# Kernel tuning notes

Measured on AMD Instinct MI355X. Metric: run time of the kernel, lower is better.

The kernel has to match this reference:

```python
import jax, jax.numpy as jnp
import numpy as np

N_WAY, K_SHOT, PRJ, D, H, W, Q = 5, 5, 14, 64, 10, 10, 1024
RATIOS = (0.25, 0.5, 0.75)
LAMDA = 32.0
MARGIN = 0.3


def _l2norm(x, axis):
    return x / jnp.maximum(jnp.linalg.norm(x, axis=axis, keepdims=True), 1e-12)


def _cos(a, b, axis=-1, eps=1e-8):
    num = (a * b).sum(axis)
    na = jnp.maximum(jnp.linalg.norm(a, axis=axis), eps)
    nb = jnp.maximum(jnp.linalg.norm(b, axis=axis), eps)
    return num / (na * nb)


def setup_inputs() -> dict:
    key = jax.random.key(0)
    ks = jax.random.split(key, 6)
    feat = jax.random.normal(ks[0], (N_WAY * K_SHOT * PRJ + Q, D, H, W), jnp.float32)
    label = jax.random.randint(ks[1], (Q,), 0, N_WAY)
    Wq = jax.random.normal(ks[2], (D, D // 4), jnp.float32) * 0.05
    bq = jnp.zeros((D // 4,), jnp.float32)
    Wk = jax.random.normal(ks[3], (D, D // 4), jnp.float32) * 0.05
    bk = jnp.zeros((D // 4,), jnp.float32)
    temperature = jnp.ones((), jnp.float32)
    gate_logits = jnp.zeros((len(RATIOS),), jnp.float32)
    return {"feat": feat, "temperature": temperature, "gate_logits": gate_logits,
            "Wq": Wq, "bq": bq, "Wk": Wk, "bk": bk, "label": label}


def reference(feat, temperature, gate_logits, Wq, bq, Wk, bk, label):
    ns = N_WAY * K_SHOT * PRJ
    support = _l2norm(feat[:ns], 1).reshape(N_WAY, K_SHOT, PRJ, D, H * W)
    query = _l2norm(feat[ns:], 1)                       # [Q, D, H, W]
    view_proto = support.mean(1)                        # [n, v, d, hw]
    q_flat = query.reshape(query.shape[0], -1)          # [Q, D*H*W]
    vf = _l2norm(view_proto.reshape(N_WAY, PRJ, -1), -1)
    # per-view similarity (vectorized over the 14-view python loop)
    sim_all = jnp.einsum('qf,nvf->qnv', q_flat, vf) / (temperature + 1e-6)
    p_w = jax.nn.softmax(sim_all, -1)                   # [Q, n, v]
    # softmax-weighted multi-view prototype fusion (replaces batched loops)
    proto_q = jnp.einsum('qnv,nvdh->qndh', p_w, view_proto)  # [Q, n, d, hw]
    spatial_attn = jax.nn.sigmoid(proto_q.mean(2, keepdims=True))
    proto_q = (proto_q * spatial_attn).sum(-1)          # [Q, n, d]
    query_vec = query.mean((2, 3))                      # [Q, d]
    # qpa align loss
    cos = _cos(query_vec[:, None, :], proto_q)          # [Q, n]
    pos_mask = jax.nn.one_hot(label, N_WAY, dtype=cos.dtype)
    pos_sim = (cos * pos_mask).sum(-1)
    neg = jnp.where(pos_mask > 0, -jnp.inf, cos)
    hardest_neg = jax.lax.top_k(neg, min(3, N_WAY - 1))[0].mean(-1)
    align_loss = jnp.maximum(hardest_neg - pos_sim + MARGIN, 0.0).mean()
    # QSA mini cross-attention
    qp = query_vec @ Wq + bq                            # [Q, D/4]
    kp = proto_q @ Wk + bk                              # [Q, n, D/4]
    scale = jnp.sqrt(jnp.asarray(D // 4, cos.dtype))
    attn = jax.nn.softmax(jnp.einsum('qe,qne->qn', qp, kp) / scale, -1)
    fused = proto_q * attn[..., None]                   # [Q, n, d]
    # DeltaGate: topk delta + multi-ratio soft mask
    base = view_proto.mean((1, 3))                      # [n, d]
    delta = jnp.abs(fused - base[None])
    Ks = [max(1, int(r * D)) for r in RATIOS]
    max_K = max(Ks)
    idx = jax.lax.top_k(delta, max_K)[1]                # [Q, n, max_K]
    mode_w = jax.nn.softmax(gate_logits)
    ranks = jnp.arange(max_K)
    rank_w = sum(mode_w[i] * (ranks < Ks[i]).astype(delta.dtype) for i in range(len(Ks)))
    combined = jnp.einsum('qnkd,k->qnd', jax.nn.one_hot(idx, D, dtype=delta.dtype), rank_w)
    gated = _l2norm(fused * combined, -1)
    cos2 = _cos(query_vec[:, None, :], gated)           # [Q, n]
    # AIS classification loss (source unavailable; faithful surrogate: scaled CE)
    logp = jax.nn.log_softmax(LAMDA * cos2, -1)
    cls_loss = -(logp * pos_mask).sum(-1).mean()
    total_loss = cls_loss + 0.3 * align_loss
    pred = jax.nn.softmax(cos2, -1)
    return pred, total_loss
```

## Files before the change

kernel.cpp:

```cpp
#include <hip/hip_runtime.h>
#include <math.h>

#define NWAY 5
#define KSHOT 5
#define PRJ 14
#define DD 64
#define PP 100
#define NQ 1024
#define NS 350
#define NPAIR 70
#define LAMDA 32.0f
#define MARGIN 0.3f
#define PCHUNK 25
#define FGROUPS 25
#define KCH 256

#define VPT_OFF   0
#define VPTS_OFF  448000
#define B2T_OFF   2688000
#define MM_OFF    3136000
#define VNINV_OFF 3143000
#define PSUM_OFF  3143128
#define QV_OFF    3147608
#define SIM32_OFF 3315544
#define PW_OFF    7903064
#define PQ4_OFF   7974744
#define CLS_OFF   9285464
#define ALN_OFF   9286488
#define PSUMP_OFF 9287512
#define SSQP_OFF  9399512
#define FQBF_OFF  9401344

#define PQ_ELEMS (NQ*NWAY*64)
#define SIM_STRIDE (NQ*NPAIR)

typedef __attribute__((ext_vector_type(8))) short short8;
typedef __attribute__((ext_vector_type(4))) float f32x4;

__device__ __forceinline__ float redsum64(float x){
  #pragma unroll
  for (int o = 1; o < 64; o <<= 1) x += __shfl_xor(x, o, 64);
  return x;
}

__device__ __forceinline__ unsigned short bfr(float x){
  unsigned int u = __float_as_uint(x);
  unsigned int r = (u + 0x7FFFu + ((u >> 16) & 1u)) >> 16;
  return (unsigned short)r;
}

__global__ __launch_bounds__(256) void kN(const float* __restrict__ feat,
                                          float* __restrict__ vptS,
                                          float* __restrict__ qv,
                                          unsigned short* __restrict__ fqb){
  __shared__ float lds[64*101];
  __shared__ float inv[100];
  int s = blockIdx.x, t = threadIdx.x;
  const float* fp = feat + (size_t)s * 6400;
  #pragma unroll
  for (int i = 0; i < 25; i++){
    int j = t + 256*i;
    int d = j / 100, p = j - d*100;
    lds[d*101 + p] = fp[j];
  }
  __syncthreads();
  if (t < 100){
    float ss = 0.f;
    #pragma unroll
    for (int d = 0; d < 64; d++){ float x = lds[d*101 + t]; ss += x*x; }
    inv[t] = 1.f / fmaxf(sqrtf(ss), 1e-12f);
  }
  __syncthreads();
  if (s < NS){
    #pragma unroll
    for (int i = 0; i < 25; i++){
      int j = t + 256*i;
      int p = j >> 6, d = j & 63;
      vptS[(size_t)s*6400 + j] = lds[d*101 + p] * inv[p];
    }
  } else {
    int q = s - NS;
    #pragma unroll
    for (int i = 0; i < 25; i++){
      int j = t + 256*i;
      int d = j / 100, p = j - d*100;
      fqb[(size_t)q*6400 + j] = bfr(lds[d*101 + p] * inv[p]);
    }
    if (t < 64){
      float sum = 0.f;
      for (int p = 0; p < PP; p++) sum += lds[t*101 + p] * inv[p];
      qv[q*64 + t] = sum * 0.01f;
    }
  }
}

__global__ __launch_bounds__(256) void kVb(const float* __restrict__ vptS,
                                           float* __restrict__ vpt,
                                           unsigned short* __restrict__ B2T,
                                           float* __restrict__ MM,
                                           float* __restrict__ psumP,
                                           float* __restrict__ ssqP){
  __shared__ float l2[256];
  __shared__ float wssq[4];
  int b = blockIdx.x;
  int pair = b / 25, jc = b - pair*25;
  int n = pair / PRJ, v = pair - n*PRJ;
  int j0 = jc * 256;
  int t = threadIdx.x;
  int j = j0 + t;
  float s = 0.f;
  #pragma unroll
  for (int k = 0; k < KSHOT; k++){
    int sk = (n*KSHOT + k)*PRJ + v;
    s += vptS[(size_t)sk*6400 + j];
  }
  float val = s * 0.2f;
  vpt[(size_t)pair*6400 + j] = val;
  int p = j >> 6, d = j & 63;
  int plocal = p & 3;
  l2[d*4 + plocal] = val;
  float sq = redsum64(val*val);
  if ((t & 63) == 0) wssq[t >> 6] = sq;
  __syncthreads();
  if (t < 64){
    int p0 = j0 >> 6;
    float4 w4 = make_float4(l2[t*4+0], l2[t*4+1], l2[t*4+2], l2[t*4+3]);
    ushort4 h;
    h.x = bfr(w4.x); h.y = bfr(w4.y); h.z = bfr(w4.z); h.w = bfr(w4.w);
    *(ushort4*)(B2T + (size_t)pair*6400 + t*100 + p0) = h;
    psumP[((size_t)pair*25 + jc)*64 + t] = w4.x + w4.y + w4.z + w4.w;
  }
  if (t >= 128 && t < 132){
    int i = t - 128;
    float m = 0.f;
    #pragma unroll
    for (int dd2 = 0; dd2 < 64; dd2++) m += l2[dd2*4 + i];
    MM[pair*100 + (j0 >> 6) + i] = m * (1.f/64.f);
  }
  if (t == 192)
    ssqP[pair*25 + jc] = wssq[0] + wssq[1] + wssq[2] + wssq[3];
}

__global__ __launch_bounds__(64) void kVc2(const float* __restrict__ psumP,
                                           const float* __restrict__ ssqP,
                                           float* __restrict__ psum,
                                           float* __restrict__ vninv){
  int pair = blockIdx.x, l = threadIdx.x;
  float s = 0.f;
  #pragma unroll
  for (int c = 0; c < 25; c++) s += psumP[((size_t)pair*25 + c)*64 + l];
  psum[pair*64 + l] = s;
  float sq = (l < 25) ? ssqP[pair*25 + l] : 0.f;
  float tot = redsum64(sq);
  if (l == 0) vninv[pair] = 1.f / fmaxf(sqrtf(tot), 1e-12f);
}

__global__ __launch_bounds__(256) void kS(const unsigned short* __restrict__ fqb,
                                          const unsigned short* __restrict__ B2T,
                                          float* __restrict__ sim32){
  int b = blockIdx.x;
  int fg = b % FGROUPS, mg = b / FGROUPS;
  int t = threadIdx.x;
  int l = t & 63;
  int wu = __builtin_amdgcn_readfirstlane(t >> 6);
  int q0 = mg*64 + wu*16;
  int fbase = fg * KCH;

  int lr = l & 15;
  int kb = l >> 4;

  f32x4 acc0 = {0.f,0.f,0.f,0.f};
  f32x4 acc1 = {0.f,0.f,0.f,0.f};
  f32x4 acc2 = {0.f,0.f,0.f,0.f};
  f32x4 acc3 = {0.f,0.f,0.f,0.f};
  f32x4 acc4 = {0.f,0.f,0.f,0.f};

  const unsigned short* Ab = fqb + (size_t)(q0 + lr)*6400 + fbase + kb*8;
  const unsigned short* Bb = B2T + (size_t)lr*6400 + fbase + kb*8;
  bool ok4 = (64 + lr) < NPAIR;

  #pragma unroll
  for (int s = 0; s < 8; s++){
    short8 a = *(const short8*)(Ab + s*32);
    short8 b0 = *(const short8*)(Bb + s*32);
    short8 b1 = *(const short8*)(Bb + 16*6400 + s*32);
    short8 b2 = *(const short8*)(Bb + 32*6400 + s*32);
    short8 b3 = *(const short8*)(Bb + 48*6400 + s*32);
    short8 b4 = ok4 ? *(const short8*)(Bb + (size_t)64*6400 + s*32) : (short8)(short)0;
    acc0 = __builtin_amdgcn_mfma_f32_16x16x32_bf16(a, b0, acc0, 0, 0, 0);
    acc1 = __builtin_amdgcn_mfma_f32_16x16x32_bf16(a, b1, acc1, 0, 0, 0);
    acc2 = __builtin_amdgcn_mfma_f32_16x16x32_bf16(a, b2, acc2, 0, 0, 0);
    acc3 = __builtin_amdgcn_mfma_f32_16x16x32_bf16(a, b3, acc3, 0, 0, 0);
    acc4 = __builtin_amdgcn_mfma_f32_16x16x32_bf16(a, b4, acc4, 0, 0, 0);
  }

  float* sp = sim32 + (size_t)fg*SIM_STRIDE + (size_t)(q0 + kb*4)*NPAIR;
  #pragma unroll
  for (int i = 0; i < 4; i++){
    sp[(size_t)i*NPAIR + lr]      = acc0[i];
    sp[(size_t)i*NPAIR + 16 + lr] = acc1[i];
    sp[(size_t)i*NPAIR + 32 + lr] = acc2[i];
    sp[(size_t)i*NPAIR + 48 + lr] = acc3[i];
    if (ok4) sp[(size_t)i*NPAIR + 64 + lr] = acc4[i];
  }
}

__global__ __launch_bounds__(256) void kM(const float* __restrict__ sim32,
                                          const float* __restrict__ vninv,
                                          const float* __restrict__ temp,
                                          float* __restrict__ pw){
  int t = blockIdx.x*256 + threadIdx.x;
  if (t >= NQ*NWAY) return;
  int q = t / NWAY, n = t - q*NWAY;
  float invT = 1.f / (temp[0] + 1e-6f);
  float s[PRJ];
  #pragma unroll
  for (int v = 0; v < PRJ; v++) s[v] = 0.f;
  for (int c = 0; c < FGROUPS; c++){
    const float* sp = sim32 + (size_t)c*SIM_STRIDE + q*NPAIR + n*PRJ;
    #pragma unroll
    for (int v = 0; v < PRJ; v++) s[v] += sp[v];
  }
  float m = -3.4e38f;
  #pragma unroll
  for (int v = 0; v < PRJ; v++){
    s[v] = s[v] * vninv[n*PRJ + v] * invT;
    m = fmaxf(m, s[v]);
  }
  float sum = 0.f;
  #pragma unroll
  for (int v = 0; v < PRJ; v++){ s[v] = expf(s[v] - m); sum += s[v]; }
  float rs = 1.f / sum;
  #pragma unroll
  for (int v = 0; v < PRJ; v++) pw[q*NPAIR + n*PRJ + v] = s[v] * rs;
}

__global__ __launch_bounds__(256) void kP(const float* __restrict__ vpt,
                                          const float* __restrict__ pw,
                                          const float* __restrict__ MM,
                                          float* __restrict__ pq4){
  __shared__ float sgl[16][PCHUNK];
  int b = blockIdx.x;
  int n  = b / 256;
  int r  = b - n*256;
  int qb = r >> 2;
  int s  = r & 3;
  int p0 = s * PCHUNK;
  int t = threadIdx.x, w = t >> 6, l = t & 63;
  int q0 = qb*16 + w*4;

  float wq[4][PRJ];
  #pragma unroll
  for (int j = 0; j < 4; j++)
    #pragma unroll
    for (int v = 0; v < PRJ; v++)
      wq[j][v] = pw[(q0+j)*NPAIR + n*PRJ + v];

  if (l < PCHUNK){
    #pragma unroll
    for (int j = 0; j < 4; j++){
      float ssg = 0.f;
      #pragma unroll
      for (int v = 0; v < PRJ; v++)
        ssg += wq[j][v] * MM[(n*PRJ + v)*100 + p0 + l];
      sgl[w*4 + j][l] = 1.f / (1.f + expf(-ssg));
    }
  }
  __syncthreads();

  float acc[4] = {0.f, 0.f, 0.f, 0.f};
  const float* vb = vpt + (size_t)n * PRJ * 6400;
  for (int pl = 0; pl < PCHUNK; pl++){
    int p = p0 + pl;
    float vv[PRJ];
    #pragma unroll
    for (int v = 0; v < PRJ; v++) vv[v] = vb[v*6400 + p*64 + l];
    #pragma unroll
    for (int j = 0; j < 4; j++){
      float dot = 0.f;
      #pragma unroll
      for (int v = 0; v < PRJ; v++) dot += wq[j][v] * vv[v];
      acc[j] += sgl[w*4 + j][pl] * dot;
    }
  }
  #pragma unroll
  for (int j = 0; j < 4; j++)
    pq4[(size_t)s*PQ_ELEMS + ((q0+j)*NWAY + n)*64 + l] = acc[j];
}

__global__ __launch_bounds__(320) void kF(const float* __restrict__ qv,
                                          const float* __restrict__ pq4,
                                          const float* __restrict__ psum,
                                          const float* __restrict__ Wq,
                                          const float* __restrict__ bq,
                                          const float* __restrict__ Wk,
                                          const float* __restrict__ bk,
                                          const float* __restrict__ gate,
                                          const int*   __restrict__ label,
                                          float* __restrict__ pred,
                                          float* __restrict__ cls,
                                          float* __restrict__ aln){
  __shared__ float qvl[64];
  __shared__ float qp[16];
  __shared__ float scn[NWAY], cosn[NWAY], c2n[NWAY];
  __shared__ float dl5[NWAY][64];
  int q = blockIdx.x, t = threadIdx.x;
  int w = t >> 6, l = t & 63;

  float qvv = qv[q*64 + l];
  float qss = redsum64(qvv*qvv);
  float qn8 = fmaxf(sqrtf(qss), 1e-8f);
  if (w == 0) qvl[l] = qvv;
  __syncthreads();
  if (w == 0 && l < 16){
    float s = bq[l];
    #pragma unroll
    for (int d = 0; d < 64; d++) s += qvl[d] * Wq[d*16 + l];
    qp[l] = s;
  }
  __syncthreads();

  float wkq = 0.f;
  #pragma unroll
  for (int e = 0; e < 16; e++) wkq += Wk[l*16 + e] * qp[e];
  float qpb = 0.f;
  #pragma unroll
  for (int e = 0; e < 16; e++) qpb += qp[e] * bk[e];

  size_t idx = (size_t)(q*NWAY + w)*64 + l;
  float x = pq4[idx] + pq4[PQ_ELEMS + idx] + pq4[2*PQ_ELEMS + idx] + pq4[3*PQ_ELEMS + idx];

  float dq = redsum64(qvv * x);
  float ps = redsum64(x * x);
  float cosw = dq / (qn8 * fmaxf(sqrtf(ps), 1e-8f));
  float sd = redsum64(x * wkq);
  float scw = (sd + qpb) * 0.25f;
  if (l == 0){ scn[w] = scw; cosn[w] = cosw; }
  __syncthreads();

  float am = scn[0];
  #pragma unroll
  for (int n = 1; n < NWAY; n++) am = fmaxf(am, scn[n]);
  float asum = 0.f;
  #pragma unroll
  for (int n = 0; n < NWAY; n++) asum += expf(scn[n] - am);
  float attw = expf(scw - am) / asum;

  float g0 = gate[0], g1 = gate[1], g2 = gate[2];
  float gm = fmaxf(fmaxf(g0, g1), g2);
  float e0 = expf(g0 - gm), e1 = expf(g1 - gm), e2 = expf(g2 - gm);
  float gs = 1.f / (e0 + e1 + e2);
  float b0 = (e0 + e1 + e2) * gs;
  float b1 = (e1 + e2) * gs;
  float b2 = e2 * gs;

  float bs = 0.f;
  #pragma unroll
  for (int v = 0; v < PRJ; v++) bs += psum[(w*PRJ + v)*64 + l];
  bs *= (1.f/1400.f);

  float f  = x * attw;
  float dd = fabsf(f - bs);
  dl5[w][l] = dd;
  int rank = 0;
  #pragma unroll 8
  for (int j = 0; j < 64; j++){
    float dj = dl5[w][j];
    rank += (dj > dd) || (dj == dd && j < l);
  }
  float cw = (rank < 16) ? b0 : (rank < 32) ? b1 : (rank < 48) ? b2 : 0.f;
  float gl = f * cw;
  float gss = redsum64(gl * gl);
  float num = redsum64(qvv * gl);
  float c2w = num / (qn8 * fmaxf(sqrtf(gss), 1e-12f));
  if (l == 0) c2n[w] = c2w;
  __syncthreads();

  float mx = c2n[0];
  #pragma unroll
  for (int n = 1; n < NWAY; n++) mx = fmaxf(mx, c2n[n]);
  float psum2 = 0.f;
  #pragma unroll
  for (int n = 0; n < NWAY; n++) psum2 += expf(c2n[n] - mx);
  if (l == 0) pred[q*NWAY + w] = expf(c2w - mx) / psum2;

  if (t == 0){
    int lab = label[q];
    float lm = LAMDA * mx;
    float lsum = 0.f;
    #pragma unroll
    for (int n = 0; n < NWAY; n++) lsum += expf(LAMDA * c2n[n] - lm);
    float c2l = c2n[lab], cosl = cosn[lab];
    float clsv = (lm + logf(lsum)) - LAMDA * c2l;
    float sum5 = 0.f, minn = 3.4e38f;
    #pragma unroll
    for (int n = 0; n < NWAY; n++){
      sum5 += cosn[n];
      if (n != lab) minn = fminf(minn, cosn[n]);
    }
    float hn = (sum5 - cosl - minn) * (1.f/3.f);
    float al = fmaxf(hn - cosl + MARGIN, 0.f);
    cls[q] = clsv; aln[q] = al;
  }
}

__global__ __launch_bounds__(256) void kL(const float* __restrict__ cls,
                                          const float* __restrict__ aln,
                                          float* __restrict__ out){
  __shared__ float r1[256], r2[256];
  int t = threadIdx.x;
  float s1 = 0.f, s2 = 0.f;
  for (int i = t; i < NQ; i += 256){ s1 += cls[i]; s2 += aln[i]; }
  r1[t] = s1; r2[t] = s2;
  __syncthreads();
  for (int o = 128; o > 0; o >>= 1){
    if (t < o){ r1[t] += r1[t + o]; r2[t] += r2[t + o]; }
    __syncthreads();
  }
  if (t == 0)
    out[NQ*NWAY] = r1[0]*(1.f/NQ) + 0.3f*(r2[0]*(1.f/NQ));
}

extern "C" void kernel_launch(void* const* d_in, const int* in_sizes, int n_in,
                              void* d_out, int out_size, void* d_ws, size_t ws_size,
                              hipStream_t stream){
  const float* feat = (const float*)d_in[0];
  const float* temp = (const float*)d_in[1];
  const float* gate = (const float*)d_in[2];
  const float* Wq   = (const float*)d_in[3];
  const float* bq   = (const float*)d_in[4];
  const float* Wk   = (const float*)d_in[5];
  const float* bk   = (const float*)d_in[6];
  const int*   lab  = (const int*)d_in[7];
  float* out = (float*)d_out;
  float* ws  = (float*)d_ws;

  float* vpt   = ws + VPT_OFF;
  float* vptS  = ws + VPTS_OFF;
  unsigned short* B2T = (unsigned short*)(ws + B2T_OFF);
  float* MMp   = ws + MM_OFF;
  float* vninv = ws + VNINV_OFF;
  float* psum  = ws + PSUM_OFF;
  float* qv    = ws + QV_OFF;
  float* sim32 = ws + SIM32_OFF;
  float* pw    = ws + PW_OFF;
  float* pq4   = ws + PQ4_OFF;
  float* cls   = ws + CLS_OFF;
  float* aln   = ws + ALN_OFF;
  float* psumP = ws + PSUMP_OFF;
  float* ssqP  = ws + SSQP_OFF;
  unsigned short* fqb = (unsigned short*)(ws + FQBF_OFF);

  hipLaunchKernelGGL(kN, dim3(NS + NQ), dim3(256), 0, stream, feat, vptS, qv, fqb);
  hipLaunchKernelGGL(kVb, dim3(NPAIR*25), dim3(256), 0, stream, vptS, vpt, B2T, MMp, psumP, ssqP);
  hipLaunchKernelGGL(kVc2, dim3(NPAIR), dim3(64), 0, stream, psumP, ssqP, psum, vninv);
  hipLaunchKernelGGL(kS, dim3(16*FGROUPS), dim3(256), 0, stream, fqb, B2T, sim32);
  hipLaunchKernelGGL(kM, dim3((NQ*NWAY + 255)/256), dim3(256), 0, stream, sim32, vninv, temp, pw);
  hipLaunchKernelGGL(kP, dim3(NWAY*256), dim3(256), 0, stream, vpt, pw, MMp, pq4);
  hipLaunchKernelGGL(kF, dim3(NQ), dim3(320), 0, stream, qv, pq4, psum, Wq, bq, Wk, bk, gate, lab, out, cls, aln);
  hipLaunchKernelGGL(kL, dim3(1), dim3(256), 0, stream, cls, aln, out);
}
```

Measured before the change: 90.92 us.

## Replace scalar prototype fusion kernel with bf16 MFMA GEMM and precomputed sigmoid gates

The scalar FP32 kP kernel, which computed softmax-weighted, sigmoid-gated prototype sums, is split into two kernels. kSg precomputes the per-query spatial sigmoid gates. kG recasts the fusion as a bf16 MFMA 16x16x32 matmul over a (view, position) reduction axis, using a new padded bf16 copy of the view prototypes (vptA) that kVb writes. The fp32 vpt buffer is dropped and partial outputs fall from 4 to 2 chunks. This trades an extra launch and a gate buffer round trip for matrix-core throughput, and adds bf16 rounding on both operands.

```diff
diff --git a/kernel.cpp b/kernel.cpp
--- a/kernel.cpp
+++ b/kernel.cpp
@@ -11,11 +11,9 @@
 #define NPAIR 70
 #define LAMDA 32.0f
 #define MARGIN 0.3f
-#define PCHUNK 25
 #define FGROUPS 25
 #define KCH 256
 
-#define VPT_OFF   0
 #define VPTS_OFF  448000
 #define B2T_OFF   2688000
 #define MM_OFF    3136000
@@ -24,12 +22,14 @@
 #define QV_OFF    3147608
 #define SIM32_OFF 3315544
 #define PW_OFF    7903064
-#define PQ4_OFF   7974744
+#define PQ2_OFF   7974744
 #define CLS_OFF   9285464
 #define ALN_OFF   9286488
 #define PSUMP_OFF 9287512
 #define SSQP_OFF  9399512
 #define FQBF_OFF  9401344
+#define VPTA_OFF  12678144
+#define SG_OFF    12964864
 
 #define PQ_ELEMS (NQ*NWAY*64)
 #define SIM_STRIDE (NQ*NPAIR)
@@ -95,8 +95,8 @@
 }
 
 __global__ __launch_bounds__(256) void kVb(const float* __restrict__ vptS,
-                                           float* __restrict__ vpt,
                                            unsigned short* __restrict__ B2T,
+                                           unsigned short* __restrict__ vptA,
                                            float* __restrict__ MM,
                                            float* __restrict__ psumP,
                                            float* __restrict__ ssqP){
@@ -115,9 +115,8 @@
     s += vptS[(size_t)sk*6400 + j];
   }
   float val = s * 0.2f;
-  vpt[(size_t)pair*6400 + j] = val;
-  int p = j >> 6, d = j & 63;
-  int plocal = p & 3;
+  int plocal = (j >> 6) & 3;
+  int d = j & 63;
   l2[d*4 + plocal] = val;
   float sq = redsum64(val*val);
   if ((t & 63) == 0) wssq[t >> 6] = sq;
@@ -128,6 +127,13 @@
     ushort4 h;
     h.x = bfr(w4.x); h.y = bfr(w4.y); h.z = bfr(w4.z); h.w = bfr(w4.w);
     *(ushort4*)(B2T + (size_t)pair*6400 + t*100 + p0) = h;
+    unsigned short* va = vptA + ((size_t)(n*64 + t))*1792 + v*128;
+    *(ushort4*)(va + p0) = h;
+    if (jc == 24){
+      #pragma unroll
+      for (int z = 0; z < 7; z++)
+        *(ushort4*)(va + 100 + z*4) = make_ushort4(0,0,0,0);
+    }
     psumP[((size_t)pair*25 + jc)*64 + t] = w4.x + w4.y + w4.z + w4.w;
   }
   if (t >= 128 && t < 132){
@@ -235,61 +241,76 @@
   for (int v = 0; v < PRJ; v++) pw[q*NPAIR + n*PRJ + v] = s[v] * rs;
 }
 
-__global__ __launch_bounds__(256) void kP(const float* __restrict__ vpt,
-                                          const float* __restrict__ pw,
-                                          const float* __restrict__ MM,
-                                          float* __restrict__ pq4){
-  __shared__ float sgl[16][PCHUNK];
-  int b = blockIdx.x;
-  int n  = b / 256;
-  int r  = b - n*256;
-  int qb = r >> 2;
-  int s  = r & 3;
-  int p0 = s * PCHUNK;
-  int t = threadIdx.x, w = t >> 6, l = t & 63;
-  int q0 = qb*16 + w*4;
-
-  float wq[4][PRJ];
-  #pragma unroll
-  for (int j = 0; j < 4; j++)
-    #pragma unroll
-    for (int v = 0; v < PRJ; v++)
-      wq[j][v] = pw[(q0+j)*NPAIR + n*PRJ + v];
-
-  if (l < PCHUNK){
-    #pragma unroll
-    for (int j = 0; j < 4; j++){
-      float ssg = 0.f;
+__global__ __launch_bounds__(256) void kSg(const float* __restrict__ pw,
+                                           const float* __restrict__ MM,
+                                           float* __restrict__ sg){
+  __shared__ float pwl[70];
+  int q = blockIdx.x, t = threadIdx.x;
+  if (t < NPAIR) pwl[t] = pw[q*NPAIR + t];
+  __syncthreads();
+  for (int i = t; i < NWAY*128; i += 256){
+    int n = i >> 7, p = i & 127;
+    float val = 0.f;
+    if (p < 100){
+      float s = 0.f;
       #pragma unroll
       for (int v = 0; v < PRJ; v++)
-        ssg += wq[j][v] * MM[(n*PRJ + v)*100 + p0 + l];
-      sgl[w*4 + j][l] = 1.f / (1.f + expf(-ssg));
-    }
-  }
-  __syncthreads();
-
-  float acc[4] = {0.f, 0.f, 0.f, 0.f};
-  const float* vb = vpt + (size_t)n * PRJ * 6400;
-  for (int pl = 0; pl < PCHUNK; pl++){
-    int p = p0 + pl;
-    float vv[PRJ];
-    #pragma unroll
-    for (int v = 0; v < PRJ; v++) vv[v] = vb[v*6400 + p*64 + l];
-    #pragma unroll
-    for (int j = 0; j < 4; j++){
-      float dot = 0.f;
-      #pragma unroll
-      for (int v = 0; v < PRJ; v++) dot += wq[j][v] * vv[v];
-      acc[j] += sgl[w*4 + j][pl] * dot;
-    }
-  }
-  #pragma unroll
-  for (int j = 0; j < 4; j++)
-    pq4[(size_t)s*PQ_ELEMS + ((q0+j)*NWAY + n)*64 + l] = acc[j];
+        s += pwl[n*PRJ + v] * MM[(n*PRJ + v)*100 + p];
+      val = 1.f / (1.f + expf(-s));
+    }
+    sg[(size_t)q*640 + i] = val;
+  }
+}
+
+__global__ __launch_bounds__(256) void kG(const float* __restrict__ sg,
+                                          const float* __restrict__ pw,
+                                          const unsigned short* __restrict__ vptA,
+                                          float* __restrict__ pq2){
+  int b = blockIdx.x;
+  int kh = b & 1;
+  int r = b >> 1;
+  int n = r / 64, qg = r - n*64;
+  int q0 = qg * 16;
+  int t = threadIdx.x;
+  int l = t & 63;
+  int wu = __builtin_amdgcn_readfirstlane(t >> 6);
+  int d0 = wu * 16;
+  int lr = l & 15, kb = l >> 4;
+
+  int q = q0 + lr;
+  const float* sgp = sg + (size_t)q*640 + n*128 + kb*8;
+  const unsigned short* Yb = vptA + ((size_t)(n*64 + d0 + lr))*1792 + kh*896 + kb*8;
+
+  float pv[7];
+  #pragma unroll
+  for (int i = 0; i < 7; i++) pv[i] = pw[q*NPAIR + n*PRJ + kh*7 + i];
+
+  f32x4 acc = {0.f,0.f,0.f,0.f};
+  #pragma unroll 4
+  for (int s = 0; s < 28; s++){
+    int pidx = (s & 3) * 32;
+    float4 g0 = *(const float4*)(sgp + pidx);
+    float4 g1 = *(const float4*)(sgp + pidx + 4);
+    float pwv = pv[s >> 2];
+    short8 a;
+    a[0] = (short)bfr(pwv * g0.x);
+    a[1] = (short)bfr(pwv * g0.y);
+    a[2] = (short)bfr(pwv * g0.z);
+    a[3] = (short)bfr(pwv * g0.w);
+    a[4] = (short)bfr(pwv * g1.x);
+    a[5] = (short)bfr(pwv * g1.y);
+    a[6] = (short)bfr(pwv * g1.z);
+    a[7] = (short)bfr(pwv * g1.w);
+    short8 y = *(const short8*)(Yb + s*32);
+    acc = __builtin_amdgcn_mfma_f32_16x16x32_bf16(a, y, acc, 0, 0, 0);
+  }
+  #pragma unroll
+  for (int i = 0; i < 4; i++)
+    pq2[(size_t)kh*PQ_ELEMS + ((size_t)(q0 + kb*4 + i)*NWAY + n)*64 + d0 + lr] = acc[i];
 }
 
 __global__ __launch_bounds__(320) void kF(const float* __restrict__ qv,
-                                          const float* __restrict__ pq4,
+                                          const float* __restrict__ pq2,
                                           const float* __restrict__ psum,
                                           const float* __restrict__ Wq,
                                           const float* __restrict__ bq,
@@ -328,7 +349,7 @@
   for (int e = 0; e < 16; e++) qpb += qp[e] * bk[e];
 
   size_t idx = (size_t)(q*NWAY + w)*64 + l;
-  float x = pq4[idx] + pq4[PQ_ELEMS + idx] + pq4[2*PQ_ELEMS + idx] + pq4[3*PQ_ELEMS + idx];
+  float x = pq2[idx] + pq2[(size_t)PQ_ELEMS + idx];
 
   float dq = redsum64(qvv * x);
   float ps = redsum64(x * x);
@@ -435,7 +456,6 @@
   float* out = (float*)d_out;
   float* ws  = (float*)d_ws;
 
-  float* vpt   = ws + VPT_OFF;
   float* vptS  = ws + VPTS_OFF;
   unsigned short* B2T = (unsigned short*)(ws + B2T_OFF);
   float* MMp   = ws + MM_OFF;
@@ -444,19 +464,22 @@
   float* qv    = ws + QV_OFF;
   float* sim32 = ws + SIM32_OFF;
   float* pw    = ws + PW_OFF;
-  float* pq4   = ws + PQ4_OFF;
+  float* pq2   = ws + PQ2_OFF;
   float* cls   = ws + CLS_OFF;
   float* aln   = ws + ALN_OFF;
   float* psumP = ws + PSUMP_OFF;
   float* ssqP  = ws + SSQP_OFF;
-  unsigned short* fqb = (unsigned short*)(ws + FQBF_OFF);
+  unsigned short* fqb  = (unsigned short*)(ws + FQBF_OFF);
+  unsigned short* vptA = (unsigned short*)(ws + VPTA_OFF);
+  float* sg    = ws + SG_OFF;
 
   hipLaunchKernelGGL(kN, dim3(NS + NQ), dim3(256), 0, stream, feat, vptS, qv, fqb);
-  hipLaunchKernelGGL(kVb, dim3(NPAIR*25), dim3(256), 0, stream, vptS, vpt, B2T, MMp, psumP, ssqP);
+  hipLaunchKernelGGL(kVb, dim3(NPAIR*25), dim3(256), 0, stream, vptS, B2T, vptA, MMp, psumP, ssqP);
   hipLaunchKernelGGL(kVc2, dim3(NPAIR), dim3(64), 0, stream, psumP, ssqP, psum, vninv);
   hipLaunchKernelGGL(kS, dim3(16*FGROUPS), dim3(256), 0, stream, fqb, B2T, sim32);
   hipLaunchKernelGGL(kM, dim3((NQ*NWAY + 255)/256), dim3(256), 0, stream, sim32, vninv, temp, pw);
-  hipLaunchKernelGGL(kP, dim3(NWAY*256), dim3(256), 0, stream, vpt, pw, MMp, pq4);
-  hipLaunchKernelGGL(kF, dim3(NQ), dim3(320), 0, stream, qv, pq4, psum, Wq, bq, Wk, bk, gate, lab, out, cls, aln);
+  hipLaunchKernelGGL(kSg, dim3(NQ), dim3(256), 0, stream, pw, MMp, sg);
+  hipLaunchKernelGGL(kG, dim3(640), dim3(256), 0, stream, sg, pw, vptA, pq2);
+  hipLaunchKernelGGL(kF, dim3(NQ), dim3(320), 0, stream, qv, pq2, psum, Wq, bq, Wk, bk, gate, lab, out, cls, aln);
   hipLaunchKernelGGL(kL, dim3(1), dim3(256), 0, stream, cls, aln, out);
 }
```

New measurement: 79.56 us, median of 2. -12.5%, faster.
